# Performance work log

Measured on AMD Instinct MI355X. Metric: run time of the kernel, lower is better.

## Reference

```python
import jax, jax.numpy as jnp
import numpy as np

EMB = 128
EDGE = 32
STEPS = 3


def _lrelu(x):
    return jax.nn.leaky_relu(x, negative_slope=0.01)


def setup_inputs() -> dict:
    key = jax.random.key(0)
    ks = jax.random.split(key, 16)
    N, E, G = 50000, 400000, 256
    x = jax.random.normal(ks[0], (N, EMB), jnp.float32)
    edge_attr = jax.random.normal(ks[1], (E, EDGE), jnp.float32)
    edge_index = jax.random.randint(ks[2], (2, E), 0, N, jnp.int64)
    batch_ind = jnp.sort(jax.random.randint(ks[3], (N,), 0, G, jnp.int64))
    data_lens = jax.random.randint(ks[4], (G,), 0, G, jnp.int64)
    s = 1.0 / np.sqrt(EMB)
    Wm = jax.random.normal(ks[5], (STEPS, EMB + EDGE, EMB), jnp.float32) * s
    bm = jnp.zeros((STEPS, EMB), jnp.float32)
    Wa = jax.random.normal(ks[6], (STEPS, 3 * EMB, EMB), jnp.float32) * s
    ba = jnp.zeros((STEPS, EMB), jnp.float32)
    Wgate = jax.random.normal(ks[7], (STEPS, EMB), jnp.float32) * s
    bgate = jnp.zeros((STEPS,), jnp.float32)
    Wfeat = jax.random.normal(ks[8], (STEPS, EMB, EMB), jnp.float32) * s
    bfeat = jnp.zeros((STEPS, EMB), jnp.float32)
    Wt = jax.random.normal(ks[9], (STEPS, 2 * EMB, EMB), jnp.float32) * s
    bt = jnp.zeros((STEPS, EMB), jnp.float32)
    return {"x": x, "edge_attr": edge_attr, "Wm": Wm, "bm": bm, "Wa": Wa,
            "ba": ba, "Wgate": Wgate, "bgate": bgate, "Wfeat": Wfeat,
            "bfeat": bfeat, "Wt": Wt, "bt": bt, "edge_index": edge_index,
            "batch_ind": batch_ind, "num_graphs": 256, "data_lens": data_lens}


def reference(x, edge_attr, Wm, bm, Wa, ba, Wgate, bgate, Wfeat, bfeat, Wt, bt,
              edge_index, batch_ind, num_graphs, data_lens):
    N = x.shape[0]
    src, dst = edge_index[0], edge_index[1]  # PyG: x_j = x[src], aggregate at dst
    xg = jnp.zeros((num_graphs, EMB), x.dtype)  # xg_init is None -> zeros
    for s in range(STEPS):
        # GraphNet: gather -> message MLP -> scatter-max -> update MLP + residual
        xg_node = xg[batch_ind]                                   # [N, emb]
        z = jnp.concatenate([x[src], edge_attr], axis=1)          # [E, emb+edge]
        m = _lrelu(z @ Wm[s] + bm[s])                             # [E, emb]
        agg = jax.ops.segment_max(m, dst, num_segments=N)         # [N, emb]
        agg = jnp.where(jnp.isneginf(agg), 0.0, agg)              # PyG fills empty with 0
        z2 = jnp.concatenate([x, xg_node, agg], axis=1)           # [N, 3*emb]
        x = _lrelu(z2 @ Wa[s] + ba[s]) + x
        # GlobalNode: segment-softmax attention pooling + transform + residual
        gate = x @ Wgate[s] + bgate[s]                            # [N]
        gmax = jax.ops.segment_max(gate, batch_ind, num_segments=num_graphs)
        gmax = jnp.where(jnp.isneginf(gmax), 0.0, gmax)
        e = jnp.exp(gate - gmax[batch_ind])
        denom = jax.ops.segment_sum(e, batch_ind, num_segments=num_graphs)
        alpha = e / denom[batch_ind]                              # [N]
        feat = _lrelu(x @ Wfeat[s] + bfeat[s])                    # [N, emb]
        pooled = jax.ops.segment_sum(alpha[:, None] * feat, batch_ind,
                                     num_segments=num_graphs)     # [G, emb]
        cat = jnp.concatenate([pooled, xg], axis=1)               # [G, 2*emb]
        xg = _lrelu(cat @ Wt[s] + bt[s]) + xg
    return x, xg
```

## Files before the change

### kernel.cpp

```cpp
#include <hip/hip_runtime.h>
#include <hip/hip_bf16.h>

#define EMB 128
#define EDGE 32
#define STEPS 3

typedef short bf8s __attribute__((ext_vector_type(8)));
typedef float f32x4 __attribute__((ext_vector_type(4)));

__device__ __forceinline__ float lrelu(float v) { return v > 0.0f ? v : 0.01f * v; }
__device__ __forceinline__ unsigned short f2bf(float f) {
    unsigned u = __float_as_uint(f);
    u += 0x7fffu + ((u >> 16) & 1u);
    return (unsigned short)(u >> 16);
}
__device__ __forceinline__ float bf2f(unsigned short s) {
    return __uint_as_float(((unsigned)s) << 16);
}
__device__ __forceinline__ unsigned pk2bf(float x, float y) {
    __hip_bfloat162 h = __float22bfloat162_rn(make_float2(x, y));
    return *(unsigned*)&h;
}

__global__ void k_hist(const int* __restrict__ dst, int E, int* __restrict__ deg) {
    int e = blockIdx.x * 256 + threadIdx.x;
    if (e < E) atomicAdd(&deg[dst[e]], 1);
}

__global__ void k_scan1(const int* __restrict__ deg, int N, int* __restrict__ rowptr,
                        int* __restrict__ bsums) {
    __shared__ int s[256];
    int t = threadIdx.x;
    int i = blockIdx.x * 256 + t;
    int v = (i < N) ? deg[i] : 0;
    s[t] = v;
    __syncthreads();
#pragma unroll
    for (int off = 1; off < 256; off <<= 1) {
        int x = (t >= off) ? s[t - off] : 0;
        __syncthreads();
        s[t] += x;
        __syncthreads();
    }
    if (i < N) rowptr[i] = s[t] - v;
    if (t == 255) bsums[blockIdx.x] = s[255];
}

__global__ void k_scan2(int* __restrict__ bsums, int NB) {
    __shared__ int s[256];
    __shared__ int carry;
    int t = threadIdx.x;
    if (t == 0) carry = 0;
    __syncthreads();
    for (int base = 0; base < NB; base += 256) {
        int i = base + t;
        int v = (i < NB) ? bsums[i] : 0;
        s[t] = v;
        __syncthreads();
#pragma unroll
        for (int off = 1; off < 256; off <<= 1) {
            int x = (t >= off) ? s[t - off] : 0;
            __syncthreads();
            s[t] += x;
            __syncthreads();
        }
        int excl = s[t] - v + carry;
        if (i < NB) bsums[i] = excl;
        int tot = s[255];
        __syncthreads();
        if (t == 0) carry += tot;
        __syncthreads();
    }
}

__global__ void k_scan3(int* __restrict__ rowptr, const int* __restrict__ bsums, int N, int E) {
    int i = blockIdx.x * 256 + threadIdx.x;
    if (i < N) rowptr[i] += bsums[i >> 8];
    if (i == 0) rowptr[N] = E;
}

__global__ void k_fill(const int* __restrict__ src, const int* __restrict__ dst,
                       const float* __restrict__ ea, int E,
                       int* __restrict__ cursor, int* __restrict__ srcp,
                       unsigned short* __restrict__ ea16p) {
    int e = blockIdx.x * 256 + threadIdx.x;
    if (e >= E) return;
    int d = dst[e];
    int p = atomicAdd(&cursor[d], 1);
    srcp[p] = src[e];
    const float4* er = (const float4*)(ea + (size_t)e * EDGE);
    union { unsigned u[16]; int4 v[4]; } o;
#pragma unroll
    for (int q = 0; q < 8; ++q) {
        float4 v = er[q];
        o.u[2 * q]     = pk2bf(v.x, v.y);
        o.u[2 * q + 1] = pk2bf(v.z, v.w);
    }
    int4* dp = (int4*)(ea16p + (size_t)p * EDGE);
#pragma unroll
    for (int q = 0; q < 4; ++q) dp[q] = o.v[q];
}

__global__ void k_hsent(unsigned short* __restrict__ h, int N) {
    h[(size_t)N * EMB + threadIdx.x] = 0xFF80u;
}

__global__ void k_gstart(const int* __restrict__ batch, int N, int G, int* __restrict__ gstart) {
    int g = blockIdx.x * blockDim.x + threadIdx.x;
    if (g > G) return;
    int lo = 0, hi = N;
    while (lo < hi) {
        int mid = (lo + hi) >> 1;
        if (batch[mid] < g) lo = mid + 1; else hi = mid;
    }
    gstart[g] = lo;
}

__global__ __launch_bounds__(256) void k_wpack(const float* __restrict__ Wm,
                                               const float* __restrict__ Wa,
                                               const float* __restrict__ Wfeat,
                                               unsigned short* __restrict__ wpack) {
    int gid = blockIdx.x * 256 + threadIdx.x;
    int unit = gid >> 14;
    int e = gid & 16383;
    int s = unit / 5, u = unit % 5;
    const float* src; int rows;
    switch (u) {
        case 0: src = Wm + (size_t)s * 160 * EMB;             rows = 128; break;
        case 1: src = Wm + (size_t)s * 160 * EMB + 128 * EMB; rows = 32;  break;
        case 2: src = Wa + (size_t)s * 384 * EMB;             rows = 128; break;
        case 3: src = Wa + (size_t)s * 384 * EMB + 256 * EMB; rows = 128; break;
        default: src = Wfeat + (size_t)s * EMB * EMB;         rows = 128; break;
    }
    int k = e >> 7, n = e & 127;
    if (k >= rows) return;
    unsigned short b = f2bf(src[(size_t)k * EMB + n]);
    int kc = k >> 5, c = n >> 4, lane = (n & 15) | (((k & 31) >> 3) << 4), j = k & 7;
    wpack[(size_t)unit * 16384 + ((size_t)(kc * 8 + c) * 64 + lane) * 8 + j] = b;
}

__device__ __forceinline__ void loadAx(const float* __restrict__ A, int row0, int wv,
                                       int lane, int N, bf8s af[4]) {
    int li = lane & 15, oct = lane >> 4;
    int m = row0 + wv * 16 + li;
    if (m >= N) m = N - 1;
    const float4* xr = (const float4*)(A + (size_t)m * EMB);
#pragma unroll
    for (int kc = 0; kc < 4; ++kc) {
        float4 a0 = xr[kc * 8 + oct * 2];
        float4 a1 = xr[kc * 8 + oct * 2 + 1];
        union { bf8s v; unsigned u[4]; } c;
        c.u[0] = pk2bf(a0.x, a0.y);
        c.u[1] = pk2bf(a0.z, a0.w);
        c.u[2] = pk2bf(a1.x, a1.y);
        c.u[3] = pk2bf(a1.z, a1.w);
        af[kc] = c.v;
    }
}
__device__ __forceinline__ void loadAa(const unsigned short* __restrict__ A16, int row0,
                                       int wv, int lane, int N, bf8s af[4]) {
    int li = lane & 15, oct = lane >> 4;
    int m = row0 + wv * 16 + li;
    if (m >= N) m = N - 1;
    const bf8s* ar = (const bf8s*)(A16 + (size_t)m * EMB);
#pragma unroll
    for (int kc = 0; kc < 4; ++kc) af[kc] = ar[kc * 4 + oct];
}
__device__ __forceinline__ void stageB(const unsigned short* __restrict__ Bp,
                                       unsigned short* lB, int tid) {
#pragma unroll
    for (int i = 0; i < 8; ++i) {
        int idx = tid + i * 256;
        ((int4*)lB)[idx] = ((const int4*)Bp)[idx];
    }
}
__device__ __forceinline__ void mfma128r(const bf8s af[4], const unsigned short* lB,
                                         f32x4 acc[8], int lane) {
#pragma unroll
    for (int kc = 0; kc < 4; ++kc) {
#pragma unroll
        for (int c = 0; c < 8; ++c) {
            bf8s b = *(const bf8s*)&lB[((kc * 8 + c) * 64 + lane) * 8];
            acc[c] = __builtin_amdgcn_mfma_f32_16x16x32_bf16(af[kc], b, acc[c], 0, 0, 0);
        }
    }
}

__global__ __launch_bounds__(256) void k_gemm_bias(const float* __restrict__ A,
                                                   const unsigned short* __restrict__ Bp,
                                                   const float* __restrict__ bias,
                                                   unsigned short* __restrict__ C, int N) {
    __shared__ unsigned short lB[16384];
    int tid = threadIdx.x, wv = tid >> 6, lane = tid & 63;
    int row0 = blockIdx.x * 64;
    stageB(Bp, lB, tid);
    bf8s af[4];
    loadAx(A, row0, wv, lane, N, af);
    __syncthreads();
    f32x4 acc[8];
#pragma unroll
    for (int c = 0; c < 8; ++c) acc[c] = (f32x4){0.f, 0.f, 0.f, 0.f};
    mfma128r(af, lB, acc, lane);
    int li = lane & 15, quad = lane >> 4;
    float bcol[8];
#pragma unroll
    for (int c = 0; c < 8; ++c) bcol[c] = bias[c * 16 + li];
#pragma unroll
    for (int rr = 0; rr < 4; ++rr) {
        int m = row0 + wv * 16 + quad * 4 + rr;
        if (m < N) {
            union { bf8s v; unsigned u[4]; } o;
#pragma unroll
            for (int j = 0; j < 4; ++j)
                o.u[j] = pk2bf(acc[2 * j][rr] + bcol[2 * j],
                               acc[2 * j + 1][rr] + bcol[2 * j + 1]);
            *(bf8s*)&C[(size_t)m * EMB + li * 8] = o.v;
        }
    }
}

__global__ __launch_bounds__(256) void k_gemm_node(const float* __restrict__ x,
                                                   const unsigned short* __restrict__ agg16,
                                                   const unsigned short* __restrict__ BpX,
                                                   const unsigned short* __restrict__ BpA,
                                                   const float* __restrict__ gb,
                                                   const int* __restrict__ batch,
                                                   float* __restrict__ xout,
                                                   const float* __restrict__ wg,
                                                   const float* __restrict__ bg,
                                                   float* __restrict__ gate, int N) {
    __shared__ unsigned short lB[16384];
    int tid = threadIdx.x, wv = tid >> 6, lane = tid & 63;
    int row0 = blockIdx.x * 64;
    stageB(BpX, lB, tid);
    bf8s af[4];
    loadAx(x, row0, wv, lane, N, af);
    __syncthreads();
    f32x4 acc[8];
#pragma unroll
    for (int c = 0; c < 8; ++c) acc[c] = (f32x4){0.f, 0.f, 0.f, 0.f};
    mfma128r(af, lB, acc, lane);
    __syncthreads();
    stageB(BpA, lB, tid);
    loadAa(agg16, row0, wv, lane, N, af);
    __syncthreads();
    mfma128r(af, lB, acc, lane);
    int li = lane & 15, quad = lane >> 4;
    float gpart[4] = {0.f, 0.f, 0.f, 0.f};
#pragma unroll
    for (int c = 0; c < 8; ++c) {
        int col = c * 16 + li;
        float wgc = wg[col];
#pragma unroll
        for (int rr = 0; rr < 4; ++rr) {
            int m = row0 + wv * 16 + quad * 4 + rr;
            if (m < N) {
                int g = batch[m];
                float b = gb[(size_t)g * EMB + col];
                float res = x[(size_t)m * EMB + col];
                float v = lrelu(acc[c][rr] + b) + res;
                xout[(size_t)m * EMB + col] = v;
                gpart[rr] = fmaf(v, wgc, gpart[rr]);
            }
        }
    }
#pragma unroll
    for (int rr = 0; rr < 4; ++rr) {
#pragma unroll
        for (int off = 1; off < 16; off <<= 1)
            gpart[rr] += __shfl_xor(gpart[rr], off, 64);
    }
    if (li == 0) {
        float b0 = bg[0];
#pragma unroll
        for (int rr = 0; rr < 4; ++rr) {
            int m = row0 + wv * 16 + quad * 4 + rr;
            if (m < N) gate[m] = gpart[rr] + b0;
        }
    }
}

__global__ __launch_bounds__(256) void k_gemm_feat(const float* __restrict__ A,
                                                   const unsigned short* __restrict__ Bp,
                                                   const float* __restrict__ bias,
                                                   const float* __restrict__ gate,
                                                   const float* __restrict__ gmax,
                                                   const float* __restrict__ denom,
                                                   const int* __restrict__ batch,
                                                   unsigned short* __restrict__ C, int N) {
    __shared__ unsigned short lB[16384];
    int tid = threadIdx.x, wv = tid >> 6, lane = tid & 63;
    int row0 = blockIdx.x * 64;
    stageB(Bp, lB, tid);
    bf8s af[4];
    loadAx(A, row0, wv, lane, N, af);
    __syncthreads();
    f32x4 acc[8];
#pragma unroll
    for (int c = 0; c < 8; ++c) acc[c] = (f32x4){0.f, 0.f, 0.f, 0.f};
    mfma128r(af, lB, acc, lane);
    int li = lane & 15, quad = lane >> 4;
    float alpha[4];
#pragma unroll
    for (int rr = 0; rr < 4; ++rr) {
        int m = row0 + wv * 16 + quad * 4 + rr;
        if (m < N) {
            int g = batch[m];
            alpha[rr] = __expf(gate[m] - gmax[g]) / denom[g];
        } else alpha[rr] = 0.f;
    }
#pragma unroll
    for (int c = 0; c < 8; ++c) {
        int col = c * 16 + li;
        float b = bias[col];
#pragma unroll
        for (int rr = 0; rr < 4; ++rr) {
            int m = row0 + wv * 16 + quad * 4 + rr;
            if (m < N) C[(size_t)m * EMB + col] = f2bf(alpha[rr] * lrelu(acc[c][rr] + b));
        }
    }
}

__global__ __launch_bounds__(256) void k_fagg(const unsigned short* __restrict__ h,
                                              const unsigned short* __restrict__ ea16p,
                                              const int* __restrict__ srcp,
                                              const int* __restrict__ rowptr,
                                              const unsigned short* __restrict__ Bp,
                                              unsigned short* __restrict__ agg, int N) {
    __shared__ unsigned short lB[4096];
    int tid = threadIdx.x;
    ((int4*)lB)[tid]       = ((const int4*)Bp)[tid];
    ((int4*)lB)[tid + 256] = ((const int4*)Bp)[tid + 256];
    __syncthreads();
    int wv = tid >> 6, lane = tid & 63;
    int n = blockIdx.x * 4 + wv;
    if (n >= N) return;
    int li = lane & 15, oct = lane >> 4;
    int r0 = rowptr[n], r1 = rowptr[n + 1], deg = r1 - r0;

    float vm[8];
#pragma unroll
    for (int ci = 0; ci < 8; ++ci) vm[ci] = -__builtin_inff();

    for (int b = 0; b < deg; b += 16) {
        int p = r0 + b + li;
        if (p > r1 - 1) p = r1 - 1;
        int srcv = srcp[p];
        bf8s a = *(const bf8s*)&ea16p[(size_t)p * EDGE + oct * 8];
        union { bf8s v; unsigned short s[8]; } hv[4];
#pragma unroll
        for (int rr = 0; rr < 4; ++rr) {
            int sr = __shfl(srcv, oct * 4 + rr, 16);
            if (b + oct * 4 + rr >= deg) sr = N;
            hv[rr].v = *(const bf8s*)&h[(size_t)sr * EMB + li * 8];
        }
#pragma unroll
        for (int ci = 0; ci < 8; ++ci) {
            bf8s bb = *(const bf8s*)&lB[(ci * 64 + lane) * 8];
            f32x4 acc;
            acc[0] = bf2f(hv[0].s[ci]);
            acc[1] = bf2f(hv[1].s[ci]);
            acc[2] = bf2f(hv[2].s[ci]);
            acc[3] = bf2f(hv[3].s[ci]);
            acc = __builtin_amdgcn_mfma_f32_16x16x32_bf16(a, bb, acc, 0, 0, 0);
#pragma unroll
            for (int rr = 0; rr < 4; ++rr) vm[ci] = fmaxf(vm[ci], acc[rr]);
        }
    }
#pragma unroll
    for (int ci = 0; ci < 8; ++ci) {
        vm[ci] = fmaxf(vm[ci], __shfl_xor(vm[ci], 16, 64));
        vm[ci] = fmaxf(vm[ci], __shfl_xor(vm[ci], 32, 64));
    }
    float s0 = (oct == 0) ? vm[0] : (oct == 1) ? vm[1] : (oct == 2) ? vm[2] : vm[3];
    float s1 = (oct == 0) ? vm[4] : (oct == 1) ? vm[5] : (oct == 2) ? vm[6] : vm[7];
    s0 = lrelu(s0);
    s1 = lrelu(s1);
    if (deg == 0) { s0 = 0.f; s1 = 0.f; }
    agg[(size_t)n * EMB + oct * 16 + li]        = f2bf(s0);
    agg[(size_t)n * EMB + (oct + 4) * 16 + li]  = f2bf(s1);
}

__global__ __launch_bounds__(128) void k_gb(const float* __restrict__ xg,
                                            const float* __restrict__ WaG,
                                            const float* __restrict__ ba,
                                            float* __restrict__ gb) {
    int g = blockIdx.x, c = threadIdx.x;
    __shared__ float row[EMB];
    row[c] = xg[(size_t)g * EMB + c];
    __syncthreads();
    float acc = ba[c];
#pragma unroll 8
    for (int k = 0; k < EMB; ++k) acc = fmaf(row[k], WaG[(size_t)k * EMB + c], acc);
    gb[(size_t)g * EMB + c] = acc;
}

__global__ __launch_bounds__(256) void k_gseg(const float* __restrict__ gate,
                                              const int* __restrict__ gstart,
                                              float* __restrict__ gmax,
                                              float* __restrict__ denom) {
    int g = blockIdx.x;
    int s0 = gstart[g], s1 = gstart[g + 1];
    __shared__ float red[256];
    int t = threadIdx.x;
    float mx = -__builtin_inff();
    for (int i = s0 + t; i < s1; i += 256) mx = fmaxf(mx, gate[i]);
    red[t] = mx;
    __syncthreads();
#pragma unroll
    for (int off = 128; off; off >>= 1) {
        if (t < off) red[t] = fmaxf(red[t], red[t + off]);
        __syncthreads();
    }
    float m = red[0];
    __syncthreads();
    float sum = 0.f;
    for (int i = s0 + t; i < s1; i += 256) sum += __expf(gate[i] - m);
    red[t] = sum;
    __syncthreads();
#pragma unroll
    for (int off = 128; off; off >>= 1) {
        if (t < off) red[t] += red[t + off];
        __syncthreads();
    }
    if (t == 0) {
        gmax[g] = (s1 > s0) ? m : 0.f;
        denom[g] = red[0];
    }
}

__global__ __launch_bounds__(512) void k_pool(const unsigned short* __restrict__ feat,
                                              const int* __restrict__ gstart,
                                              float* __restrict__ pooled) {
    int g = blockIdx.x;
    int c = threadIdx.x & 127;
    int r = threadIdx.x >> 7;
    int s0 = gstart[g], s1 = gstart[g + 1];
    float s = 0.f;
    for (int i = s0 + r; i < s1; i += 4) s += bf2f(feat[(size_t)i * EMB + c]);
    __shared__ float red[512];
    red[threadIdx.x] = s;
    __syncthreads();
    if (threadIdx.x < 256) red[threadIdx.x] += red[threadIdx.x + 256];
    __syncthreads();
    if (threadIdx.x < 128)
        pooled[(size_t)g * EMB + threadIdx.x] = red[threadIdx.x] + red[threadIdx.x + 128];
}

__global__ __launch_bounds__(128) void k_xg(const float* __restrict__ pooled,
                                            const float* __restrict__ xg,
                                            const float* __restrict__ Wt,
                                            const float* __restrict__ bt,
                                            float* __restrict__ xg_out) {
    int g = blockIdx.x, c = threadIdx.x;
    __shared__ float row[256];
    row[c] = pooled[(size_t)g * EMB + c];
    row[c + 128] = xg[(size_t)g * EMB + c];
    __syncthreads();
    float acc = bt[c];
#pragma unroll 8
    for (int k = 0; k < 256; ++k) acc = fmaf(row[k], Wt[(size_t)k * EMB + c], acc);
    xg_out[(size_t)g * EMB + c] = lrelu(acc) + row[c + 128];
}

extern "C" void kernel_launch(void* const* d_in, const int* in_sizes, int n_in,
                              void* d_out, int out_size, void* d_ws, size_t ws_size,
                              hipStream_t stream) {
    const float* x0    = (const float*)d_in[0];
    const float* ea    = (const float*)d_in[1];
    const float* Wm    = (const float*)d_in[2];
    const float* bm    = (const float*)d_in[3];
    const float* Wa    = (const float*)d_in[4];
    const float* ba    = (const float*)d_in[5];
    const float* Wgate = (const float*)d_in[6];
    const float* bgate = (const float*)d_in[7];
    const float* Wfeat = (const float*)d_in[8];
    const float* bfeat = (const float*)d_in[9];
    const float* Wt    = (const float*)d_in[10];
    const float* bt    = (const float*)d_in[11];
    const int*   eidx  = (const int*)d_in[12];
    const int*   batch = (const int*)d_in[13];

    int N = in_sizes[0] / EMB;
    int E = in_sizes[1] / EDGE;
    int G = in_sizes[15];

    char* w = (char*)d_ws;
    auto alloc = [&](size_t bytes) {
        char* p = w;
        w += (bytes + 255) & ~(size_t)255;
        return p;
    };
    unsigned short* h16   = (unsigned short*)alloc((size_t)(N + 1) * EMB * 2);
    unsigned short* agg16 = (unsigned short*)alloc((size_t)N * EMB * 2);
    unsigned short* ft16  = (unsigned short*)alloc((size_t)N * EMB * 2);
    float* gate   = (float*)alloc((size_t)N * 4);
    float* gb     = (float*)alloc((size_t)G * EMB * 4);
    float* pooled = (float*)alloc((size_t)G * EMB * 4);
    float* gmax   = (float*)alloc((size_t)G * 4);
    float* denom  = (float*)alloc((size_t)G * 4);
    float* xg_a   = (float*)alloc((size_t)G * EMB * 4);
    float* xg_b   = (float*)alloc((size_t)G * EMB * 4);
    int* deg      = (int*)alloc((size_t)N * 4);
    int* rowptr   = (int*)alloc((size_t)(N + 1) * 4);
    int* cursor   = (int*)alloc((size_t)N * 4);
    int* srcp     = (int*)alloc((size_t)E * 4);
    unsigned short* ea16p = (unsigned short*)alloc((size_t)E * EDGE * 2);
    int* gstart   = (int*)alloc((size_t)(G + 1) * 4);
    int* bsums    = (int*)alloc(1024 * 4);
    unsigned short* wpack = (unsigned short*)alloc((size_t)15 * 16384 * 2);

    const int* esrc = eidx;
    const int* edst = eidx + E;
    int ebl = (E + 255) / 256;
    int NB  = (N + 255) / 256;

    hipMemsetAsync(deg, 0, (size_t)N * 4, stream);
    k_hist<<<ebl, 256, 0, stream>>>(edst, E, deg);
    k_scan1<<<NB, 256, 0, stream>>>(deg, N, rowptr, bsums);
    k_scan2<<<1, 256, 0, stream>>>(bsums, NB);
    k_scan3<<<NB, 256, 0, stream>>>(rowptr, bsums, N, E);
    hipMemcpyAsync(cursor, rowptr, (size_t)N * 4, hipMemcpyDeviceToDevice, stream);
    k_fill<<<ebl, 256, 0, stream>>>(esrc, edst, ea, E, cursor, srcp, ea16p);
    k_hsent<<<1, 128, 0, stream>>>(h16, N);
    k_gstart<<<(G + 256) / 256, 256, 0, stream>>>(batch, N, G, gstart);
    hipMemsetAsync(xg_a, 0, (size_t)G * EMB * 4, stream);
    k_wpack<<<960, 256, 0, stream>>>(Wm, Wa, Wfeat, wpack);

    int gemm_blocks = (N + 63) / 64;
    int fagg_blocks = (N + 3) / 4;

    const float* x_in = x0;
    float* xg_cur = xg_a;
    float* xg_nxt = xg_b;

    for (int s = 0; s < STEPS; ++s) {
        const unsigned short* wp = wpack + (size_t)s * 5 * 16384;
        float* x_out = (s == STEPS - 1) ? (float*)d_out : (float*)x_in;

        k_gemm_bias<<<gemm_blocks, 256, 0, stream>>>(x_in, wp + 0 * 16384, bm + s * EMB,
                                                     h16, N);
        k_fagg<<<fagg_blocks, 256, 0, stream>>>(h16, ea16p, srcp, rowptr, wp + 1 * 16384,
                                                agg16, N);
        k_gb<<<G, 128, 0, stream>>>(xg_cur, Wa + (size_t)s * 384 * EMB + 128 * EMB,
                                    ba + s * EMB, gb);
        k_gemm_node<<<gemm_blocks, 256, 0, stream>>>(x_in, agg16, wp + 2 * 16384,
                                                     wp + 3 * 16384, gb, batch, x_out,
                                                     Wgate + s * EMB, bgate + s, gate, N);
        k_gseg<<<G, 256, 0, stream>>>(gate, gstart, gmax, denom);
        k_gemm_feat<<<gemm_blocks, 256, 0, stream>>>(x_out, wp + 4 * 16384, bfeat + s * EMB,
                                                     gate, gmax, denom, batch, ft16, N);
        k_pool<<<G, 512, 0, stream>>>(ft16, gstart, pooled);
        k_xg<<<G, 128, 0, stream>>>(pooled, xg_cur, Wt + (size_t)s * 256 * EMB,
                                    bt + s * EMB, xg_nxt);

        x_in = x_out;
        float* tmp = xg_cur; xg_cur = xg_nxt; xg_nxt = tmp;
    }

    hipMemcpyAsync((float*)d_out + (size_t)N * EMB, xg_cur, (size_t)G * EMB * 4,
                   hipMemcpyDeviceToDevice, stream);
}
```

Before: 596.8 us.

## Fuse attention pooling into feat GEMM via atomics and fold gb into xg update

The feat GEMM epilogue now accumulates alpha-weighted features straight into pooled with atomics, using a wave-level shuffle reduction when all 16 rows of a wave belong to one graph. This removes the bf16 feat buffer write and the separate pooling kernel. The gb computation for the next step is folded into k_xg, and for step 0 it reduces to the bias because xg starts at zero. Edge-attribute permutation is split out of the atomic fill into a separate coalesced-by-destination kernel. The atomics make pooling summation order nondeterministic, and the fill step adds an extra index array.

```diff
diff --git a/kernel.cpp b/kernel.cpp
--- a/kernel.cpp
+++ b/kernel.cpp
@@ -79,16 +79,24 @@
     if (i == 0) rowptr[N] = E;
 }
 
-__global__ void k_fill(const int* __restrict__ src, const int* __restrict__ dst,
-                       const float* __restrict__ ea, int E,
-                       int* __restrict__ cursor, int* __restrict__ srcp,
-                       unsigned short* __restrict__ ea16p) {
+__global__ void k_fill(const int* __restrict__ src, const int* __restrict__ dst, int E,
+                       int* __restrict__ cursor, int2* __restrict__ sp2) {
     int e = blockIdx.x * 256 + threadIdx.x;
     if (e >= E) return;
     int d = dst[e];
     int p = atomicAdd(&cursor[d], 1);
-    srcp[p] = src[e];
-    const float4* er = (const float4*)(ea + (size_t)e * EDGE);
+    sp2[p] = make_int2(src[e], e);
+}
+
+__global__ __launch_bounds__(256) void k_eaperm(const float* __restrict__ ea,
+                                                const int2* __restrict__ sp2,
+                                                unsigned short* __restrict__ ea16p,
+                                                int* __restrict__ srcp, int E) {
+    int p = blockIdx.x * 256 + threadIdx.x;
+    if (p >= E) return;
+    int2 sp = sp2[p];
+    srcp[p] = sp.x;
+    const float4* er = (const float4*)(ea + (size_t)sp.y * EDGE);
     union { unsigned u[16]; int4 v[4]; } o;
 #pragma unroll
     for (int q = 0; q < 8; ++q) {
@@ -103,6 +111,10 @@
 
 __global__ void k_hsent(unsigned short* __restrict__ h, int N) {
     h[(size_t)N * EMB + threadIdx.x] = 0xFF80u;
+}
+
+__global__ void k_gb0(const float* __restrict__ ba, float* __restrict__ gb) {
+    gb[(size_t)blockIdx.x * EMB + threadIdx.x] = ba[threadIdx.x];
 }
 
 __global__ void k_gstart(const int* __restrict__ batch, int N, int G, int* __restrict__ gstart) {
@@ -287,7 +299,7 @@
                                                    const float* __restrict__ gmax,
                                                    const float* __restrict__ denom,
                                                    const int* __restrict__ batch,
-                                                   unsigned short* __restrict__ C, int N) {
+                                                   float* __restrict__ pooled, int N) {
     __shared__ unsigned short lB[16384];
     int tid = threadIdx.x, wv = tid >> 6, lane = tid & 63;
     int row0 = blockIdx.x * 64;
@@ -300,24 +312,106 @@
     for (int c = 0; c < 8; ++c) acc[c] = (f32x4){0.f, 0.f, 0.f, 0.f};
     mfma128r(af, lB, acc, lane);
     int li = lane & 15, quad = lane >> 4;
+    int rb = row0 + wv * 16;
+    if (rb >= N) return;
     float alpha[4];
+    int grow[4];
 #pragma unroll
     for (int rr = 0; rr < 4; ++rr) {
-        int m = row0 + wv * 16 + quad * 4 + rr;
+        int m = rb + quad * 4 + rr;
         if (m < N) {
             int g = batch[m];
+            grow[rr] = g;
             alpha[rr] = __expf(gate[m] - gmax[g]) / denom[g];
-        } else alpha[rr] = 0.f;
-    }
+        } else { alpha[rr] = 0.f; grow[rr] = 0; }
+    }
+    int gs = batch[rb];
+    int mlast = rb + 15; if (mlast >= N) mlast = N - 1;
+    bool uni = (gs == batch[mlast]);
 #pragma unroll
     for (int c = 0; c < 8; ++c) {
         int col = c * 16 + li;
         float b = bias[col];
-#pragma unroll
-        for (int rr = 0; rr < 4; ++rr) {
-            int m = row0 + wv * 16 + quad * 4 + rr;
-            if (m < N) C[(size_t)m * EMB + col] = f2bf(alpha[rr] * lrelu(acc[c][rr] + b));
-        }
+        float v0 = alpha[0] * lrelu(acc[c][0] + b);
+        float v1 = alpha[1] * lrelu(acc[c][1] + b);
+        float v2 = alpha[2] * lrelu(acc[c][2] + b);
+        float v3 = alpha[3] * lrelu(acc[c][3] + b);
+        if (uni) {
+            float s = (v0 + v1) + (v2 + v3);
+            s += __shfl_xor(s, 16, 64);
+            s += __shfl_xor(s, 32, 64);
+            if (quad == 0) atomicAdd(&pooled[(size_t)gs * EMB + col], s);
+        } else {
+            if (rb + quad * 4 + 0 < N) atomicAdd(&pooled[(size_t)grow[0] * EMB + col], v0);
+            if (rb + quad * 4 + 1 < N) atomicAdd(&pooled[(size_t)grow[1] * EMB + col], v1);
+            if (rb + quad * 4 + 2 < N) atomicAdd(&pooled[(size_t)grow[2] * EMB + col], v2);
+            if (rb + quad * 4 + 3 < N) atomicAdd(&pooled[(size_t)grow[3] * EMB + col], v3);
+        }
+    }
+}
+
+__global__ __launch_bounds__(256) void k_gseg(const float* __restrict__ gate,
+                                              const int* __restrict__ gstart,
+                                              float* __restrict__ gmax,
+                                              float* __restrict__ denom,
+                                              float* __restrict__ pooled) {
+    int g = blockIdx.x;
+    int t = threadIdx.x;
+    if (t < EMB) pooled[(size_t)g * EMB + t] = 0.f;
+    int s0 = gstart[g], s1 = gstart[g + 1];
+    __shared__ float red[256];
+    float mx = -__builtin_inff();
+    for (int i = s0 + t; i < s1; i += 256) mx = fmaxf(mx, gate[i]);
+    red[t] = mx;
+    __syncthreads();
+#pragma unroll
+    for (int off = 128; off; off >>= 1) {
+        if (t < off) red[t] = fmaxf(red[t], red[t + off]);
+        __syncthreads();
+    }
+    float m = red[0];
+    __syncthreads();
+    float sum = 0.f;
+    for (int i = s0 + t; i < s1; i += 256) sum += __expf(gate[i] - m);
+    red[t] = sum;
+    __syncthreads();
+#pragma unroll
+    for (int off = 128; off; off >>= 1) {
+        if (t < off) red[t] += red[t + off];
+        __syncthreads();
+    }
+    if (t == 0) {
+        gmax[g] = (s1 > s0) ? m : 0.f;
+        denom[g] = red[0];
+    }
+}
+
+__global__ __launch_bounds__(128) void k_xg(const float* __restrict__ pooled,
+                                            const float* __restrict__ xg,
+                                            const float* __restrict__ Wt,
+                                            const float* __restrict__ bt,
+                                            float* __restrict__ xg_out,
+                                            const float* __restrict__ WaGn,
+                                            const float* __restrict__ ban,
+                                            float* __restrict__ gb) {
+    int g = blockIdx.x, c = threadIdx.x;
+    __shared__ float row[256];
+    row[c] = pooled[(size_t)g * EMB + c];
+    row[c + 128] = xg[(size_t)g * EMB + c];
+    __syncthreads();
+    float acc = bt[c];
+#pragma unroll 8
+    for (int k = 0; k < 256; ++k) acc = fmaf(row[k], Wt[(size_t)k * EMB + c], acc);
+    float v = lrelu(acc) + row[c + 128];
+    xg_out[(size_t)g * EMB + c] = v;
+    if (WaGn) {
+        __syncthreads();
+        row[c] = v;
+        __syncthreads();
+        float a2 = ban[c];
+#pragma unroll 8
+        for (int k = 0; k < EMB; ++k) a2 = fmaf(row[k], WaGn[(size_t)k * EMB + c], a2);
+        gb[(size_t)g * EMB + c] = a2;
     }
 }
 
@@ -379,88 +473,6 @@
     if (deg == 0) { s0 = 0.f; s1 = 0.f; }
     agg[(size_t)n * EMB + oct * 16 + li]        = f2bf(s0);
     agg[(size_t)n * EMB + (oct + 4) * 16 + li]  = f2bf(s1);
-}
-
-__global__ __launch_bounds__(128) void k_gb(const float* __restrict__ xg,
-                                            const float* __restrict__ WaG,
-                                            const float* __restrict__ ba,
-                                            float* __restrict__ gb) {
-    int g = blockIdx.x, c = threadIdx.x;
-    __shared__ float row[EMB];
-    row[c] = xg[(size_t)g * EMB + c];
-    __syncthreads();
-    float acc = ba[c];
-#pragma unroll 8
-    for (int k = 0; k < EMB; ++k) acc = fmaf(row[k], WaG[(size_t)k * EMB + c], acc);
-    gb[(size_t)g * EMB + c] = acc;
-}
-
-__global__ __launch_bounds__(256) void k_gseg(const float* __restrict__ gate,
-                                              const int* __restrict__ gstart,
-                                              float* __restrict__ gmax,
-                                              float* __restrict__ denom) {
-    int g = blockIdx.x;
-    int s0 = gstart[g], s1 = gstart[g + 1];
-    __shared__ float red[256];
-    int t = threadIdx.x;
-    float mx = -__builtin_inff();
-    for (int i = s0 + t; i < s1; i += 256) mx = fmaxf(mx, gate[i]);
-    red[t] = mx;
-    __syncthreads();
-#pragma unroll
-    for (int off = 128; off; off >>= 1) {
-        if (t < off) red[t] = fmaxf(red[t], red[t + off]);
-        __syncthreads();
-    }
-    float m = red[0];
-    __syncthreads();
-    float sum = 0.f;
-    for (int i = s0 + t; i < s1; i += 256) sum += __expf(gate[i] - m);
-    red[t] = sum;
-    __syncthreads();
-#pragma unroll
-    for (int off = 128; off; off >>= 1) {
-        if (t < off) red[t] += red[t + off];
-        __syncthreads();
-    }
-    if (t == 0) {
-        gmax[g] = (s1 > s0) ? m : 0.f;
-        denom[g] = red[0];
-    }
-}
-
-__global__ __launch_bounds__(512) void k_pool(const unsigned short* __restrict__ feat,
-                                              const int* __restrict__ gstart,
-                                              float* __restrict__ pooled) {
-    int g = blockIdx.x;
-    int c = threadIdx.x & 127;
-    int r = threadIdx.x >> 7;
-    int s0 = gstart[g], s1 = gstart[g + 1];
-    float s = 0.f;
-    for (int i = s0 + r; i < s1; i += 4) s += bf2f(feat[(size_t)i * EMB + c]);
-    __shared__ float red[512];
-    red[threadIdx.x] = s;
-    __syncthreads();
-    if (threadIdx.x < 256) red[threadIdx.x] += red[threadIdx.x + 256];
-    __syncthreads();
-    if (threadIdx.x < 128)
-        pooled[(size_t)g * EMB + threadIdx.x] = red[threadIdx.x] + red[threadIdx.x + 128];
-}
-
-__global__ __launch_bounds__(128) void k_xg(const float* __restrict__ pooled,
-                                            const float* __restrict__ xg,
-                                            const float* __restrict__ Wt,
-                                            const float* __restrict__ bt,
-                                            float* __restrict__ xg_out) {
-    int g = blockIdx.x, c = threadIdx.x;
-    __shared__ float row[256];
-    row[c] = pooled[(size_t)g * EMB + c];
-    row[c + 128] = xg[(size_t)g * EMB + c];
-    __syncthreads();
-    float acc = bt[c];
-#pragma unroll 8
-    for (int k = 0; k < 256; ++k) acc = fmaf(row[k], Wt[(size_t)k * EMB + c], acc);
-    xg_out[(size_t)g * EMB + c] = lrelu(acc) + row[c + 128];
 }
 
 extern "C" void kernel_launch(void* const* d_in, const int* in_sizes, int n_in,
@@ -493,7 +505,6 @@
     };
     unsigned short* h16   = (unsigned short*)alloc((size_t)(N + 1) * EMB * 2);
     unsigned short* agg16 = (unsigned short*)alloc((size_t)N * EMB * 2);
-    unsigned short* ft16  = (unsigned short*)alloc((size_t)N * EMB * 2);
     float* gate   = (float*)alloc((size_t)N * 4);
     float* gb     = (float*)alloc((size_t)G * EMB * 4);
     float* pooled = (float*)alloc((size_t)G * EMB * 4);
@@ -504,6 +515,7 @@
     int* deg      = (int*)alloc((size_t)N * 4);
     int* rowptr   = (int*)alloc((size_t)(N + 1) * 4);
     int* cursor   = (int*)alloc((size_t)N * 4);
+    int2* sp2     = (int2*)alloc((size_t)E * 8);
     int* srcp     = (int*)alloc((size_t)E * 4);
     unsigned short* ea16p = (unsigned short*)alloc((size_t)E * EDGE * 2);
     int* gstart   = (int*)alloc((size_t)(G + 1) * 4);
@@ -521,8 +533,10 @@
     k_scan2<<<1, 256, 0, stream>>>(bsums, NB);
     k_scan3<<<NB, 256, 0, stream>>>(rowptr, bsums, N, E);
     hipMemcpyAsync(cursor, rowptr, (size_t)N * 4, hipMemcpyDeviceToDevice, stream);
-    k_fill<<<ebl, 256, 0, stream>>>(esrc, edst, ea, E, cursor, srcp, ea16p);
+    k_fill<<<ebl, 256, 0, stream>>>(esrc, edst, E, cursor, sp2);
+    k_eaperm<<<ebl, 256, 0, stream>>>(ea, sp2, ea16p, srcp, E);
     k_hsent<<<1, 128, 0, stream>>>(h16, N);
+    k_gb0<<<G, 128, 0, stream>>>(ba, gb);
     k_gstart<<<(G + 256) / 256, 256, 0, stream>>>(batch, N, G, gstart);
     hipMemsetAsync(xg_a, 0, (size_t)G * EMB * 4, stream);
     k_wpack<<<960, 256, 0, stream>>>(Wm, Wa, Wfeat, wpack);
@@ -542,17 +556,17 @@
                                                      h16, N);
         k_fagg<<<fagg_blocks, 256, 0, stream>>>(h16, ea16p, srcp, rowptr, wp + 1 * 16384,
                                                 agg16, N);
-        k_gb<<<G, 128, 0, stream>>>(xg_cur, Wa + (size_t)s * 384 * EMB + 128 * EMB,
-                                    ba + s * EMB, gb);
         k_gemm_node<<<gemm_blocks, 256, 0, stream>>>(x_in, agg16, wp + 2 * 16384,
                                                      wp + 3 * 16384, gb, batch, x_out,
                                                      Wgate + s * EMB, bgate + s, gate, N);
-        k_gseg<<<G, 256, 0, stream>>>(gate, gstart, gmax, denom);
+        k_gseg<<<G, 256, 0, stream>>>(gate, gstart, gmax, denom, pooled);
         k_gemm_feat<<<gemm_blocks, 256, 0, stream>>>(x_out, wp + 4 * 16384, bfeat + s * EMB,
-                                                     gate, gmax, denom, batch, ft16, N);
-        k_pool<<<G, 512, 0, stream>>>(ft16, gstart, pooled);
+                                                     gate, gmax, denom, batch, pooled, N);
+        const float* WaGn = (s < STEPS - 1) ? Wa + (size_t)(s + 1) * 384 * EMB + 128 * EMB
+                                            : nullptr;
+        const float* ban  = (s < STEPS - 1) ? ba + (s + 1) * EMB : nullptr;
         k_xg<<<G, 128, 0, stream>>>(pooled, xg_cur, Wt + (size_t)s * 256 * EMB,
-                                    bt + s * EMB, xg_nxt);
+                                    bt + s * EMB, xg_nxt, WaGn, ban, gb);
 
         x_in = x_out;
         float* tmp = xg_cur; xg_cur = xg_nxt; xg_nxt = tmp;
```

After: 559.6 us. 1.07x faster.
